# Kernel optimization log

Hardware: AMD Instinct MI355X
Metric: run time of the kernel (lower is better)

The kernel has to match this reference:

```python
import jax, jax.numpy as jnp
import numpy as np

B, S, D, H = 2, 2048, 1024, 8
DH = D // H          # hidden_dim == attn_dim == 128
TOTAL = 4 * D        # (2*hidden_dim + 2*attn_dim) * H
EPS = 1e-5
ROPE_BASE = 10000.0


def _layernorm(x, g, b):
    m = jnp.mean(x, axis=-1, keepdims=True)
    v = jnp.mean(jnp.square(x - m), axis=-1, keepdims=True)
    return (x - m) * jax.lax.rsqrt(v + EPS) * g + b


def _rope(x):
    # x: [B, H, S, DH], interleaved even/odd RoPE as in the torch module
    half = DH // 2
    inv_freq = 1.0 / (ROPE_BASE ** (jnp.arange(0, DH, 2, dtype=jnp.float32) / DH))  # [half]
    t = jnp.arange(x.shape[2], dtype=jnp.float32)
    freqs = t[:, None] * inv_freq[None, :]                 # [S, half]
    cos = jnp.cos(freqs)[None, None, :, :]                 # [1,1,S,half]
    sin = jnp.sin(freqs)[None, None, :, :]
    xe, xo = x[..., 0::2], x[..., 1::2]
    re = xe * cos - xo * sin
    ro = xe * sin + xo * cos
    return jnp.stack([re, ro], axis=-1).reshape(x.shape)


def setup_inputs() -> dict:
    key = jax.random.key(0)
    ks = jax.random.split(key, 6)
    x = jax.random.normal(ks[0], (B, S, D), dtype=jnp.float32)
    attention_mask = jnp.ones((B, S), dtype=bool)
    # weights stored [in, out] so forward is x @ W + b
    w_uvqk = 0.02 * jax.random.normal(ks[1], (D, TOTAL), dtype=jnp.float32)
    b_uvqk = jnp.zeros((TOTAL,), dtype=jnp.float32)
    w_out = 0.02 * jax.random.normal(ks[2], (3 * D, D), dtype=jnp.float32)
    b_out = jnp.zeros((D,), dtype=jnp.float32)
    ln1_g = jnp.ones((D,), dtype=jnp.float32)
    ln1_b = jnp.zeros((D,), dtype=jnp.float32)
    ln2_g = jnp.ones((D,), dtype=jnp.float32)
    ln2_b = jnp.zeros((D,), dtype=jnp.float32)
    return {"x": x, "attention_mask": attention_mask,
            "ln1_g": ln1_g, "ln1_b": ln1_b,
            "w_uvqk": w_uvqk, "b_uvqk": b_uvqk,
            "ln2_g": ln2_g, "ln2_b": ln2_b,
            "w_out": w_out, "b_out": b_out}


def reference(x, attention_mask, ln1_g, ln1_b, w_uvqk, b_uvqk, ln2_g, ln2_b, w_out, b_out):
    normed = _layernorm(x, ln1_g, ln1_b)
    uvqk = jax.nn.silu(normed @ w_uvqk + b_uvqk)          # [B,S,4D]
    u, v, q, k = jnp.split(uvqk, [D, 2 * D, 3 * D], axis=-1)
    q = q.reshape(B, S, H, DH).transpose(0, 2, 1, 3)      # [B,H,S,DH]
    k = k.reshape(B, S, H, DH).transpose(0, 2, 1, 3)
    v = v.reshape(B, S, H, DH).transpose(0, 2, 1, 3)
    q, k = _rope(q), _rope(k)
    scale = jnp.float32(DH) ** 0.5
    scores = jnp.einsum('bhsd,bhtd->bhst', q, k) / scale  # [B,H,S,S] fp32
    causal = jnp.tril(jnp.ones((S, S), dtype=bool))
    pad = attention_mask[:, None, :, None] & attention_mask[:, None, None, :]
    valid = pad & causal[None, None, :, :]
    scores = jnp.where(valid, scores, jnp.float32(-30.0))
    scores = jnp.clip(scores, -30.0, 30.0)
    attn = jax.nn.silu(scores)                            # SiLU instead of softmax
    ao = jnp.einsum('bhst,bhtd->bhsd', attn, v)           # [B,H,S,DH]
    ao = ao.transpose(0, 2, 1, 3).reshape(B, S, D)
    normed_attn = _layernorm(ao, ln2_g, ln2_b)
    cat = jnp.concatenate([u, ao, normed_attn * u], axis=-1)  # [B,S,3D]
    return x + (cat @ w_out + b_out)
```

## Files before the change

kernel.cpp:

```cpp
#include <hip/hip_runtime.h>
#include <hip/hip_bf16.h>
#include <math.h>

#define Bm 2
#define Sm 2048
#define Dm 1024
#define Hm 8
#define DHm 128
#define TOTALm 4096
#define ROWS (Bm*Sm)
#define K2m (3*Dm)

typedef __bf16 bf16;
typedef __bf16 bf16x8 __attribute__((ext_vector_type(8)));
typedef __bf16 bf16x4 __attribute__((ext_vector_type(4)));
typedef float  f32x4  __attribute__((ext_vector_type(4)));

__device__ __forceinline__ void stage_tile_128x32(
    const bf16* __restrict__ g, int ld, bf16* lds, int tid)
{
    int wid = tid >> 6;
    #pragma unroll
    for (int j = 0; j < 2; j++) {
        int e0  = (j*256 + tid) * 8;
        int row = e0 >> 5, col = e0 & 31;
        const bf16* src = g + (size_t)row*ld + col;
        bf16* dst = lds + (size_t)(j*256 + wid*64)*8;
        __builtin_amdgcn_global_load_lds(
            (const __attribute__((address_space(1))) unsigned int*)src,
            (__attribute__((address_space(3))) unsigned int*)dst,
            16, 0, 0);
    }
}

__device__ __forceinline__ void stage_tile_64x32(
    const bf16* __restrict__ g, int ld, bf16* lds, int tid)
{
    int wid = tid >> 6;
    int e0 = tid * 8;
    int row = e0 >> 5, col = e0 & 31;
    const bf16* src = g + (size_t)row*ld + col;
    bf16* dst = lds + (size_t)wid*512;
    __builtin_amdgcn_global_load_lds(
        (const __attribute__((address_space(1))) unsigned int*)src,
        (__attribute__((address_space(3))) unsigned int*)dst,
        16, 0, 0);
}

__global__ __launch_bounds__(256) void ln1_kernel(
    const float* __restrict__ x, const float* __restrict__ g,
    const float* __restrict__ bb, bf16* __restrict__ out)
{
    int row = blockIdx.x;
    const float* xr = x + (size_t)row * Dm;
    int tid = threadIdx.x;
    float4 v = *(const float4*)(xr + tid*4);
    float s = v.x+v.y+v.z+v.w;
    for (int o=32;o>0;o>>=1) s += __shfl_down(s,o);
    __shared__ float red[4]; __shared__ float stats[2];
    int wid = tid>>6, lane = tid&63;
    if (lane==0) red[wid]=s;
    __syncthreads();
    if (tid==0) stats[0] = (red[0]+red[1]+red[2]+red[3]) * (1.f/Dm);
    __syncthreads();
    float m = stats[0];
    float d0=v.x-m,d1=v.y-m,d2=v.z-m,d3=v.w-m;
    float q = d0*d0+d1*d1+d2*d2+d3*d3;
    for (int o=32;o>0;o>>=1) q += __shfl_down(q,o);
    if (lane==0) red[wid]=q;
    __syncthreads();
    if (tid==0) stats[1] = rsqrtf((red[0]+red[1]+red[2]+red[3])*(1.f/Dm) + 1e-5f);
    __syncthreads();
    float rs = stats[1];
    float4 gv = *(const float4*)(g + tid*4);
    float4 bv = *(const float4*)(bb + tid*4);
    bf16x4 o;
    o[0] = (bf16)(d0*rs*gv.x + bv.x);
    o[1] = (bf16)(d1*rs*gv.y + bv.y);
    o[2] = (bf16)(d2*rs*gv.z + bv.z);
    o[3] = (bf16)(d3*rs*gv.w + bv.w);
    *(bf16x4*)(out + (size_t)row*Dm + tid*4) = o;
}

__global__ __launch_bounds__(256) void transpose_kernel(
    const float* __restrict__ in, bf16* __restrict__ out, int R, int C)
{
    __shared__ float tile[32][33];
    int c0 = blockIdx.x*32, r0 = blockIdx.y*32;
    int tx = threadIdx.x & 31, ty = threadIdx.x >> 5;
    for (int i=0;i<4;i++) {
        int r = ty + i*8;
        tile[r][tx] = in[(size_t)(r0+r)*C + c0+tx];
    }
    __syncthreads();
    for (int i=0;i<4;i++) {
        int cl = ty + i*8;
        out[(size_t)(c0+cl)*R + r0+tx] = (bf16)tile[tx][cl];
    }
}

__global__ __launch_bounds__(256) void rope_table_kernel(float* __restrict__ ct, float* __restrict__ st)
{
    int idx = blockIdx.x*256 + threadIdx.x;
    int t = idx >> 6, p = idx & 63;
    float inv = expf(-0.143911568f * (float)p);
    float f = (float)t * inv;
    float sv, cv;
    sincosf(f, &sv, &cv);
    ct[idx] = cv; st[idx] = sv;
}

__global__ __launch_bounds__(256,4) void gemm1_kernel(
    const bf16* __restrict__ A, const bf16* __restrict__ Bt,
    const float* __restrict__ bias,
    const float* __restrict__ ct, const float* __restrict__ st,
    bf16* __restrict__ cat, bf16* __restrict__ qb, bf16* __restrict__ kb,
    bf16* __restrict__ vt)
{
    __shared__ __align__(16) bf16 sm[17408];
    const int K = Dm;
    int m0 = blockIdx.y*128, n0 = blockIdx.x*128;
    int tid = threadIdx.x, wid = tid>>6, lane = tid&63;
    int quad = lane>>4, l16 = lane&15;
    int wm = (wid>>1)*64, wn = (wid&1)*64;
    f32x4 acc[4][4] = {};
    bf16* sA = sm;
    bf16* sB = sm + 8192;
    for (int k0=0;k0<K;k0+=64) {
        __syncthreads();
        stage_tile_128x32(A  + (size_t)m0*K + k0,      K, sA,        tid);
        stage_tile_128x32(A  + (size_t)m0*K + k0 + 32, K, sA + 4096, tid);
        stage_tile_128x32(Bt + (size_t)n0*K + k0,      K, sB,        tid);
        stage_tile_128x32(Bt + (size_t)n0*K + k0 + 32, K, sB + 4096, tid);
        __syncthreads();
        #pragma unroll
        for (int kc=0;kc<2;kc++) {
            bf16x8 af[4], bfr[4];
            #pragma unroll
            for (int t=0;t<4;t++) af[t]  = *(const bf16x8*)&sA[kc*4096 + (wm+t*16+l16)*32 + quad*8];
            #pragma unroll
            for (int t=0;t<4;t++) bfr[t] = *(const bf16x8*)&sB[kc*4096 + (wn+t*16+l16)*32 + quad*8];
            #pragma unroll
            for (int tm=0;tm<4;tm++)
                #pragma unroll
                for (int tn=0;tn<4;tn++)
                    acc[tm][tn] = __builtin_amdgcn_mfma_f32_16x16x32_bf16(af[tm], bfr[tn], acc[tm][tn], 0,0,0);
        }
    }
    int sect = n0 >> 10;
    if (sect == 1) {
        __syncthreads();
        #pragma unroll
        for (int tm=0;tm<4;tm++)
        #pragma unroll
        for (int tn=0;tn<4;tn++) {
            int colg = n0 + wn + tn*16 + l16;
            float bval = bias[colg];
            int d = colg & 127;
            #pragma unroll
            for (int r=0;r<4;r++) {
                int srow = wm + tm*16 + quad*4 + r;
                float val = acc[tm][tn][r] + bval;
                val = val / (1.f + __expf(-val));
                sm[d*136 + srow] = (bf16)val;
            }
        }
        __syncthreads();
        int h = (n0 >> 7) & 7;
        int b = m0 >> 11, s0l = m0 & 2047;
        int d2 = tid >> 1, sh = (tid & 1)*64;
        bf16* dst = vt + ((size_t)(b*Hm+h)*DHm + d2)*Sm + s0l + sh;
        const bf16* srcl = &sm[d2*136 + sh];
        #pragma unroll
        for (int i=0;i<8;i++)
            *(bf16x8*)(dst + i*8) = *(const bf16x8*)(srcl + i*8);
    } else if (sect == 0) {
        #pragma unroll
        for (int tm=0;tm<4;tm++)
        #pragma unroll
        for (int tn=0;tn<4;tn++) {
            int c = n0 + wn + tn*16 + l16;
            float bval = bias[c];
            #pragma unroll
            for (int r=0;r<4;r++) {
                int row = m0 + wm + tm*16 + quad*4 + r;
                float val = acc[tm][tn][r] + bval;
                val = val / (1.f + __expf(-val));
                cat[(size_t)row*K2m + c] = (bf16)val;
            }
        }
    } else {
        bf16* dstb = (sect==2) ? qb : kb;
        float postscale = (sect==2) ? 0.08838834764831845f : 1.0f;
        #pragma unroll
        for (int tm=0;tm<4;tm++)
        #pragma unroll
        for (int tn=0;tn<4;tn++) {
            int colg = n0 + wn + tn*16 + l16;
            int c = colg & 1023;
            int h = c>>7, d = c&127, p = d>>1;
            float bval = bias[colg];
            #pragma unroll
            for (int r=0;r<4;r++) {
                int row = m0 + wm + tm*16 + quad*4 + r;
                float val = acc[tm][tn][r] + bval;
                val = val / (1.f + __expf(-val));
                int b = row>>11, s = row&2047;
                float pv = __shfl_xor(val, 1);
                float cv = ct[s*64+p], sv = st[s*64+p];
                float res = (d&1) ? (pv*sv + val*cv) : (val*cv - pv*sv);
                dstb[((size_t)(b*Hm+h)*Sm + s)*DHm + d] = (bf16)(res * postscale);
            }
        }
    }
}

__global__ __launch_bounds__(256,3) void attn_kernel(
    const bf16* __restrict__ qb, const bf16* __restrict__ kb,
    const bf16* __restrict__ vt, float* __restrict__ ao)
{
    __shared__ __align__(16) bf16 sK[16384];
    __shared__ __align__(16) bf16 P[64*136];
    int bid = blockIdx.x;
    int qt = (bid < 256) ? (31 - (bid >> 4)) : ((bid - 256) >> 4);
    int head = bid & 15;
    int b = head >> 3, h = head & 7;
    const size_t headoff = (size_t)(b*Hm+h)*Sm*DHm;
    const bf16* Q  = qb + headoff;
    const bf16* Km = kb + headoff;
    const bf16* V  = vt + headoff;
    int tid=threadIdx.x, wid=tid>>6, lane=tid&63, quad=lane>>4, l16=lane&15;
    int wm=(wid>>1)*32, wn=(wid&1)*64;
    int q0 = qt*64;
    int nkt = (qt>>1) + 1;
    f32x4 accO[2][4] = {};
    bf16x8 qf[4][2];
    #pragma unroll
    for (int kc=0;kc<4;kc++)
        #pragma unroll
        for (int t=0;t<2;t++)
            qf[kc][t] = *(const bf16x8*)(Q + (size_t)(q0+wm+t*16+l16)*DHm + kc*32 + quad*8);
    for (int kt=0; kt<nkt; kt++) {
        int t0 = kt*128;
        __syncthreads();
        #pragma unroll
        for (int kc=0;kc<4;kc++)
            stage_tile_128x32(Km + (size_t)t0*DHm + kc*32, DHm, sK + kc*4096, tid);
        __syncthreads();
        f32x4 accS[2][4] = {};
        #pragma unroll
        for (int kc=0;kc<4;kc++) {
            bf16x8 bfr[4];
            #pragma unroll
            for (int t=0;t<4;t++) bfr[t] = *(const bf16x8*)&sK[kc*4096 + (wn+t*16+l16)*32 + quad*8];
            #pragma unroll
            for (int tm=0;tm<2;tm++)
                #pragma unroll
                for (int tn=0;tn<4;tn++)
                    accS[tm][tn] = __builtin_amdgcn_mfma_f32_16x16x32_bf16(qf[kc][tm], bfr[tn], accS[tm][tn], 0,0,0);
        }
        if (t0 + 127 <= q0) {
            #pragma unroll
            for (int tm=0;tm<2;tm++)
            #pragma unroll
            for (int tn=0;tn<4;tn++)
                #pragma unroll
                for (int r=0;r<4;r++) {
                    int srow = wm+tm*16+quad*4+r;
                    int tcol = wn+tn*16+l16;
                    float s = fminf(30.f, fmaxf(-30.f, accS[tm][tn][r]));
                    float p = s * __builtin_amdgcn_rcpf(1.f + __expf(-s));
                    P[srow*136 + tcol] = (bf16)p;
                }
        } else {
            #pragma unroll
            for (int tm=0;tm<2;tm++)
            #pragma unroll
            for (int tn=0;tn<4;tn++)
                #pragma unroll
                for (int r=0;r<4;r++) {
                    int srow = wm+tm*16+quad*4+r;
                    int tcol = wn+tn*16+l16;
                    float s = fminf(30.f, fmaxf(-30.f, accS[tm][tn][r]));
                    float p = (t0+tcol > q0+srow) ? 0.f
                              : s * __builtin_amdgcn_rcpf(1.f + __expf(-s));
                    P[srow*136 + tcol] = (bf16)p;
                }
        }
        __syncthreads();
        int kcn = ((q0 + 63 - t0) >> 5) + 1;
        if (kcn > 4) kcn = 4;
        for (int kc=0;kc<kcn;kc++) {
            bf16x8 af[2], bfr[4];
            #pragma unroll
            for (int t=0;t<2;t++) af[t]  = *(const bf16x8*)&P[(wm+t*16+l16)*136 + kc*32 + quad*8];
            #pragma unroll
            for (int t=0;t<4;t++) bfr[t] = *(const bf16x8*)(V + (size_t)(wn+t*16+l16)*Sm + t0 + kc*32 + quad*8);
            #pragma unroll
            for (int tm=0;tm<2;tm++)
                #pragma unroll
                for (int tn=0;tn<4;tn++)
                    accO[tm][tn] = __builtin_amdgcn_mfma_f32_16x16x32_bf16(af[tm], bfr[tn], accO[tm][tn], 0,0,0);
        }
    }
    #pragma unroll
    for (int tm=0;tm<2;tm++)
    #pragma unroll
    for (int tn=0;tn<4;tn++)
        #pragma unroll
        for (int r=0;r<4;r++) {
            int s = q0+wm+tm*16+quad*4+r;
            int d = wn+tn*16+l16;
            ao[((size_t)(b*Sm+s))*Dm + h*DHm + d] = accO[tm][tn][r];
        }
}

__global__ __launch_bounds__(256) void ln2_cat_kernel(
    const float* __restrict__ ao, const float* __restrict__ g,
    const float* __restrict__ bb, bf16* __restrict__ cat)
{
    int row = blockIdx.x;
    const float* ar = ao + (size_t)row * Dm;
    int tid = threadIdx.x;
    float4 v = *(const float4*)(ar + tid*4);
    float s = v.x+v.y+v.z+v.w;
    for (int o=32;o>0;o>>=1) s += __shfl_down(s,o);
    __shared__ float red[4]; __shared__ float stats[2];
    int wid = tid>>6, lane = tid&63;
    if (lane==0) red[wid]=s;
    __syncthreads();
    if (tid==0) stats[0] = (red[0]+red[1]+red[2]+red[3]) * (1.f/Dm);
    __syncthreads();
    float m = stats[0];
    float d0=v.x-m,d1=v.y-m,d2=v.z-m,d3=v.w-m;
    float q = d0*d0+d1*d1+d2*d2+d3*d3;
    for (int o=32;o>0;o>>=1) q += __shfl_down(q,o);
    if (lane==0) red[wid]=q;
    __syncthreads();
    if (tid==0) stats[1] = rsqrtf((red[0]+red[1]+red[2]+red[3])*(1.f/Dm) + 1e-5f);
    __syncthreads();
    float rs = stats[1];
    float4 gv = *(const float4*)(g + tid*4);
    float4 bv = *(const float4*)(bb + tid*4);
    bf16* crow = cat + (size_t)row * K2m;
    bf16x4 u4 = *(const bf16x4*)(crow + tid*4);
    bf16x4 a4, nu4;
    a4[0]=(bf16)v.x; a4[1]=(bf16)v.y; a4[2]=(bf16)v.z; a4[3]=(bf16)v.w;
    nu4[0]=(bf16)(((v.x-m)*rs*gv.x+bv.x) * (float)u4[0]);
    nu4[1]=(bf16)(((v.y-m)*rs*gv.y+bv.y) * (float)u4[1]);
    nu4[2]=(bf16)(((v.z-m)*rs*gv.z+bv.z) * (float)u4[2]);
    nu4[3]=(bf16)(((v.w-m)*rs*gv.w+bv.w) * (float)u4[3]);
    *(bf16x4*)(crow + 1024 + tid*4) = a4;
    *(bf16x4*)(crow + 2048 + tid*4) = nu4;
}

__global__ __launch_bounds__(256,4) void gemm2_kernel(
    const bf16* __restrict__ A, const bf16* __restrict__ Bt,
    const float* __restrict__ bias, const float* __restrict__ x,
    float* __restrict__ out)
{
    __shared__ __align__(16) bf16 sm[12288];
    const int K = K2m, N = Dm;
    int m0 = blockIdx.y*128, n0 = blockIdx.x*64;
    int tid = threadIdx.x, wid = tid>>6, lane = tid&63;
    int quad = lane>>4, l16 = lane&15;
    int wm = (wid>>1)*64, wn = (wid&1)*32;
    f32x4 acc[4][2] = {};
    bf16* sA = sm;
    bf16* sB = sm + 8192;
    for (int k0=0;k0<K;k0+=64) {
        __syncthreads();
        stage_tile_128x32(A  + (size_t)m0*K + k0,      K, sA,        tid);
        stage_tile_128x32(A  + (size_t)m0*K + k0 + 32, K, sA + 4096, tid);
        stage_tile_64x32 (Bt + (size_t)n0*K + k0,      K, sB,        tid);
        stage_tile_64x32 (Bt + (size_t)n0*K + k0 + 32, K, sB + 2048, tid);
        __syncthreads();
        #pragma unroll
        for (int kc=0;kc<2;kc++) {
            bf16x8 af[4], bfr[2];
            #pragma unroll
            for (int t=0;t<4;t++) af[t]  = *(const bf16x8*)&sA[kc*4096 + (wm+t*16+l16)*32 + quad*8];
            #pragma unroll
            for (int t=0;t<2;t++) bfr[t] = *(const bf16x8*)&sB[kc*2048 + (wn+t*16+l16)*32 + quad*8];
            #pragma unroll
            for (int tm=0;tm<4;tm++)
                #pragma unroll
                for (int tn=0;tn<2;tn++)
                    acc[tm][tn] = __builtin_amdgcn_mfma_f32_16x16x32_bf16(af[tm], bfr[tn], acc[tm][tn], 0,0,0);
        }
    }
    #pragma unroll
    for (int tm=0;tm<4;tm++)
    #pragma unroll
    for (int tn=0;tn<2;tn++) {
        int col = n0 + wn + tn*16 + l16;
        float bval = bias[col];
        #pragma unroll
        for (int r=0;r<4;r++) {
            int row = m0 + wm + tm*16 + quad*4 + r;
            out[(size_t)row*N + col] = acc[tm][tn][r] + bval + x[(size_t)row*N + col];
        }
    }
}

extern "C" void kernel_launch(void* const* d_in, const int* in_sizes, int n_in,
                              void* d_out, int out_size, void* d_ws, size_t ws_size,
                              hipStream_t stream)
{
    const float* x      = (const float*)d_in[0];
    const float* ln1_g  = (const float*)d_in[2];
    const float* ln1_b  = (const float*)d_in[3];
    const float* w_uvqk = (const float*)d_in[4];
    const float* b_uvqk = (const float*)d_in[5];
    const float* ln2_g  = (const float*)d_in[6];
    const float* ln2_b  = (const float*)d_in[7];
    const float* w_out  = (const float*)d_in[8];
    const float* b_out  = (const float*)d_in[9];

    char* w = (char*)d_ws;
    bf16*  normed = (bf16*)(w);
    bf16*  Wt1    = (bf16*)(w + 8388608);
    bf16*  Wt2    = (bf16*)(w + 16777216);
    bf16*  qb     = (bf16*)(w + 23068672);
    bf16*  kb     = (bf16*)(w + 31457280);
    bf16*  vt     = (bf16*)(w + 39845888);
    float* ao     = (float*)(w + 48234496);
    bf16*  cat    = (bf16*)(w + 65011712);
    float* ct     = (float*)(w + 90177536);
    float* st     = (float*)(w + 90701824);

    ln1_kernel<<<ROWS, 256, 0, stream>>>(x, ln1_g, ln1_b, normed);
    transpose_kernel<<<dim3(TOTALm/32, Dm/32), 256, 0, stream>>>(w_uvqk, Wt1, Dm, TOTALm);
    transpose_kernel<<<dim3(Dm/32, K2m/32), 256, 0, stream>>>(w_out, Wt2, K2m, Dm);
    rope_table_kernel<<<(Sm*64)/256, 256, 0, stream>>>(ct, st);
    gemm1_kernel<<<dim3(TOTALm/128, ROWS/128), 256, 0, stream>>>(
        normed, Wt1, b_uvqk, ct, st, cat, qb, kb, vt);
    attn_kernel<<<512, 256, 0, stream>>>(qb, kb, vt, ao);
    ln2_cat_kernel<<<ROWS, 256, 0, stream>>>(ao, ln2_g, ln2_b, cat);
    gemm2_kernel<<<dim3(Dm/64, ROWS/128), 256, 0, stream>>>(
        cat, Wt2, b_out, x, (float*)d_out);
}
```

Baseline: 279.2 us.

## Split long causal attention tiles over key range and drop K LDS staging

Query tiles in the upper half of the sequence now have their key loop split across two blocks, so the grid grows to 768 blocks and per-block work is more even. The second half's partial output goes to a separate zero-initialised buffer that the LN2 kernel adds in. K fragments are now read straight from global memory instead of being staged in shared memory. P is double-buffered, which removes two barriers per key tile. In exchange it adds a 16 MB memset, an extra partial-output read in LN2, and a reliance on cache hits for the uncoalesced global K reads.

```diff
diff --git a/kernel.cpp b/kernel.cpp
--- a/kernel.cpp
+++ b/kernel.cpp
@@ -217,14 +217,27 @@
 
 __global__ __launch_bounds__(256,3) void attn_kernel(
     const bf16* __restrict__ qb, const bf16* __restrict__ kb,
-    const bf16* __restrict__ vt, float* __restrict__ ao)
-{
-    __shared__ __align__(16) bf16 sK[16384];
-    __shared__ __align__(16) bf16 P[64*136];
+    const bf16* __restrict__ vt, float* __restrict__ ao0,
+    float* __restrict__ ao1)
+{
+    __shared__ __align__(16) bf16 P[2*64*136];
     int bid = blockIdx.x;
-    int qt = (bid < 256) ? (31 - (bid >> 4)) : ((bid - 256) >> 4);
     int head = bid & 15;
+    int idx = bid >> 4;
     int b = head >> 3, h = head & 7;
+    int qt, k_begin, k_end;
+    float* aoOut;
+    if (idx < 32) {
+        qt = 31 - (idx >> 1);
+        int nkt = (qt >> 1) + 1;
+        int half = (nkt + 1) >> 1;
+        if ((idx & 1) == 0) { k_begin = 0;    k_end = half; aoOut = ao0; }
+        else                { k_begin = half; k_end = nkt;  aoOut = ao1; }
+    } else {
+        qt = 47 - idx;
+        k_begin = 0; k_end = (qt >> 1) + 1;
+        aoOut = ao0;
+    }
     const size_t headoff = (size_t)(b*Hm+h)*Sm*DHm;
     const bf16* Q  = qb + headoff;
     const bf16* Km = kb + headoff;
@@ -232,7 +245,6 @@
     int tid=threadIdx.x, wid=tid>>6, lane=tid&63, quad=lane>>4, l16=lane&15;
     int wm=(wid>>1)*32, wn=(wid&1)*64;
     int q0 = qt*64;
-    int nkt = (qt>>1) + 1;
     f32x4 accO[2][4] = {};
     bf16x8 qf[4][2];
     #pragma unroll
@@ -240,19 +252,17 @@
         #pragma unroll
         for (int t=0;t<2;t++)
             qf[kc][t] = *(const bf16x8*)(Q + (size_t)(q0+wm+t*16+l16)*DHm + kc*32 + quad*8);
-    for (int kt=0; kt<nkt; kt++) {
+    int it = 0;
+    for (int kt=k_begin; kt<k_end; kt++, it++) {
         int t0 = kt*128;
-        __syncthreads();
-        #pragma unroll
-        for (int kc=0;kc<4;kc++)
-            stage_tile_128x32(Km + (size_t)t0*DHm + kc*32, DHm, sK + kc*4096, tid);
-        __syncthreads();
+        bf16* Pb = P + (it & 1) * 8704;
         f32x4 accS[2][4] = {};
         #pragma unroll
         for (int kc=0;kc<4;kc++) {
             bf16x8 bfr[4];
             #pragma unroll
-            for (int t=0;t<4;t++) bfr[t] = *(const bf16x8*)&sK[kc*4096 + (wn+t*16+l16)*32 + quad*8];
+            for (int t=0;t<4;t++)
+                bfr[t] = *(const bf16x8*)(Km + (size_t)(t0+wn+t*16+l16)*DHm + kc*32 + quad*8);
             #pragma unroll
             for (int tm=0;tm<2;tm++)
                 #pragma unroll
@@ -270,7 +280,7 @@
                     int tcol = wn+tn*16+l16;
                     float s = fminf(30.f, fmaxf(-30.f, accS[tm][tn][r]));
                     float p = s * __builtin_amdgcn_rcpf(1.f + __expf(-s));
-                    P[srow*136 + tcol] = (bf16)p;
+                    Pb[srow*136 + tcol] = (bf16)p;
                 }
         } else {
             #pragma unroll
@@ -284,7 +294,7 @@
                     float s = fminf(30.f, fmaxf(-30.f, accS[tm][tn][r]));
                     float p = (t0+tcol > q0+srow) ? 0.f
                               : s * __builtin_amdgcn_rcpf(1.f + __expf(-s));
-                    P[srow*136 + tcol] = (bf16)p;
+                    Pb[srow*136 + tcol] = (bf16)p;
                 }
         }
         __syncthreads();
@@ -293,7 +303,7 @@
         for (int kc=0;kc<kcn;kc++) {
             bf16x8 af[2], bfr[4];
             #pragma unroll
-            for (int t=0;t<2;t++) af[t]  = *(const bf16x8*)&P[(wm+t*16+l16)*136 + kc*32 + quad*8];
+            for (int t=0;t<2;t++) af[t]  = *(const bf16x8*)&Pb[(wm+t*16+l16)*136 + kc*32 + quad*8];
             #pragma unroll
             for (int t=0;t<4;t++) bfr[t] = *(const bf16x8*)(V + (size_t)(wn+t*16+l16)*Sm + t0 + kc*32 + quad*8);
             #pragma unroll
@@ -311,18 +321,20 @@
         for (int r=0;r<4;r++) {
             int s = q0+wm+tm*16+quad*4+r;
             int d = wn+tn*16+l16;
-            ao[((size_t)(b*Sm+s))*Dm + h*DHm + d] = accO[tm][tn][r];
+            aoOut[((size_t)(b*Sm+s))*Dm + h*DHm + d] = accO[tm][tn][r];
         }
 }
 
 __global__ __launch_bounds__(256) void ln2_cat_kernel(
-    const float* __restrict__ ao, const float* __restrict__ g,
+    const float* __restrict__ ao0, const float* __restrict__ ao1,
+    const float* __restrict__ g,
     const float* __restrict__ bb, bf16* __restrict__ cat)
 {
     int row = blockIdx.x;
-    const float* ar = ao + (size_t)row * Dm;
     int tid = threadIdx.x;
-    float4 v = *(const float4*)(ar + tid*4);
+    float4 v  = *(const float4*)(ao0 + (size_t)row*Dm + tid*4);
+    float4 v1 = *(const float4*)(ao1 + (size_t)row*Dm + tid*4);
+    v.x += v1.x; v.y += v1.y; v.z += v1.z; v.w += v1.w;
     float s = v.x+v.y+v.z+v.w;
     for (int o=32;o>0;o>>=1) s += __shfl_down(s,o);
     __shared__ float red[4]; __shared__ float stats[2];
@@ -424,10 +436,11 @@
     bf16*  qb     = (bf16*)(w + 23068672);
     bf16*  kb     = (bf16*)(w + 31457280);
     bf16*  vt     = (bf16*)(w + 39845888);
-    float* ao     = (float*)(w + 48234496);
+    float* ao0    = (float*)(w + 48234496);
     bf16*  cat    = (bf16*)(w + 65011712);
     float* ct     = (float*)(w + 90177536);
     float* st     = (float*)(w + 90701824);
+    float* ao1    = (float*)(w);
 
     ln1_kernel<<<ROWS, 256, 0, stream>>>(x, ln1_g, ln1_b, normed);
     transpose_kernel<<<dim3(TOTALm/32, Dm/32), 256, 0, stream>>>(w_uvqk, Wt1, Dm, TOTALm);
@@ -435,8 +448,9 @@
     rope_table_kernel<<<(Sm*64)/256, 256, 0, stream>>>(ct, st);
     gemm1_kernel<<<dim3(TOTALm/128, ROWS/128), 256, 0, stream>>>(
         normed, Wt1, b_uvqk, ct, st, cat, qb, kb, vt);
-    attn_kernel<<<512, 256, 0, stream>>>(qb, kb, vt, ao);
-    ln2_cat_kernel<<<ROWS, 256, 0, stream>>>(ao, ln2_g, ln2_b, cat);
+    hipMemsetAsync(ao1, 0, (size_t)ROWS*Dm*sizeof(float), stream);
+    attn_kernel<<<768, 256, 0, stream>>>(qb, kb, vt, ao0, ao1);
+    ln2_cat_kernel<<<ROWS, 256, 0, stream>>>(ao0, ao1, ln2_g, ln2_b, cat);
     gemm2_kernel<<<dim3(Dm/64, ROWS/128), 256, 0, stream>>>(
         cat, Wt2, b_out, x, (float*)d_out);
 }
```

Measured after the change: 300.8 us. 1.08x slower.
